# Kernel tuning notes

Hardware: AMD Instinct MI355X
Metric: run time of the kernel (lower is better)

## Reference

```python
import jax, jax.numpy as jnp
import numpy as np

T, B, N = 5, 1048576, 16
GAMMA = 0.99


def setup_inputs() -> dict:
    key = jax.random.key(0)
    k = jax.random.split(key, 6)
    q = jax.random.normal(k[0], (B, N), dtype=jnp.float32)
    next_n_q = jax.random.normal(k[1], (B, N), dtype=jnp.float32)
    action = jax.random.randint(k[2], (B,), 0, N)
    next_n_action = jax.random.randint(k[3], (B,), 0, N)
    reward = jax.random.normal(k[4], (T, B), dtype=jnp.float32)
    done = jax.random.randint(k[5], (B,), 0, 2).astype(jnp.bool_)
    weight = jnp.ones((B,), dtype=jnp.float32)
    gamma = jnp.float32(GAMMA)
    return {"q": q, "next_n_q": next_n_q, "action": action,
            "next_n_action": next_n_action, "reward": reward,
            "done": done, "weight": weight, "gamma": gamma}


def reference(q, next_n_q, action, next_n_action, reward, done, weight, gamma):
    # q, next_n_q: (B, N); action/next_n_action/done/weight: (B,); reward: (T, B)
    t = reward.shape[0]
    # gather Q(s,a) and Q(s_{t+n}, a') by action index
    q_s_a = jnp.take_along_axis(q, action[:, None], axis=1)[:, 0]            # (B,)
    next_q_s_a = jnp.take_along_axis(next_n_q, next_n_action[:, None], axis=1)[:, 0]
    # n-step discounted return: sum_t gamma^t r_t + gamma^T * Q' * (1 - done)
    factors = gamma ** jnp.arange(t, dtype=q.dtype)                          # (T,)
    not_done = 1.0 - done.astype(q.dtype)
    target = jnp.einsum('t,tb->b', factors, reward) + (gamma ** t) * next_q_s_a * not_done
    target = jax.lax.stop_gradient(target)
    # per-sample MSE td error, weighted mean loss
    td_error_per_sample = jnp.square(q_s_a - target)                         # (B,)
    loss = jnp.mean(td_error_per_sample * weight)                            # ()
    return loss, td_error_per_sample
```

## Files before the change

### kernel.cpp

```cpp
#include <hip/hip_runtime.h>


#define TILE_ROWS 512
#define BLOCK     256

__global__ __launch_bounds__(BLOCK) void qnstep_td_main(
    const float* __restrict__ q,
    const float* __restrict__ nq,
    const int*   __restrict__ act,
    const int*   __restrict__ nact,
    const float* __restrict__ rew,
    const int*   __restrict__ done,
    const float* __restrict__ w,
    const float* __restrict__ gamma_p,
    float*       __restrict__ out,
    float*       __restrict__ partial,
    int B, int T)
{
    __shared__ float tile[TILE_ROWS * 16];

    const int tid  = threadIdx.x;
    const long long base = (long long)blockIdx.x * TILE_ROWS;
    const float gamma = gamma_p[0];

    const long long g = base / 2 + tid;
    const int2   a2  = ((const int2*)act)[g];
    const int2   na2 = ((const int2*)nact)[g];
    const int2   d2  = ((const int2*)done)[g];
    const float2 w2  = ((const float2*)w)[g];

    float t0 = 0.f, t1 = 0.f, f = 1.0f;
    #pragma unroll 8
    for (int t = 0; t < T; ++t) {
        const float2 r2 = ((const float2*)(rew + (long long)t * B))[g];
        t0 += f * r2.x; t1 += f * r2.y;
        f *= gamma;
    }

    const int s0 = tid * 2, s1 = tid * 2 + 1;

    float4* t4 = (float4*)tile;
    {
        const float4* q4 = (const float4*)q + base * 4;
        #pragma unroll
        for (int j = 0; j < 8; ++j)
            t4[tid + j * BLOCK] = q4[tid + j * BLOCK];
    }
    __syncthreads();
    const float qa0 = tile[s0 * 16 + a2.x];
    const float qa1 = tile[s1 * 16 + a2.y];
    __syncthreads();

    {
        const float4* nq4 = (const float4*)nq + base * 4;
        #pragma unroll
        for (int j = 0; j < 8; ++j)
            t4[tid + j * BLOCK] = nq4[tid + j * BLOCK];
    }
    __syncthreads();
    const float nqa0 = tile[s0 * 16 + na2.x];
    const float nqa1 = tile[s1 * 16 + na2.y];

    t0 += f * nqa0 * (d2.x ? 0.f : 1.f);
    t1 += f * nqa1 * (d2.y ? 0.f : 1.f);
    const float e0 = qa0 - t0, e1 = qa1 - t1;
    const float td0 = e0 * e0, td1 = e1 * e1;

    out[1 + base + s0] = td0;
    out[1 + base + s1] = td1;

    float val = td0 * w2.x + td1 * w2.y;

    #pragma unroll
    for (int off = 32; off > 0; off >>= 1)
        val += __shfl_down(val, off, 64);

    __shared__ float ssum[BLOCK / 64];
    const int wave = tid >> 6, lane = tid & 63;
    if (lane == 0) ssum[wave] = val;
    __syncthreads();
    if (tid == 0) {
        float s = 0.f;
        #pragma unroll
        for (int i = 0; i < BLOCK / 64; ++i) s += ssum[i];
        partial[blockIdx.x] = s;
    }
}

__global__ __launch_bounds__(256) void qnstep_td_generic(
    const float* __restrict__ q, const float* __restrict__ nq,
    const int* __restrict__ act, const int* __restrict__ nact,
    const float* __restrict__ rew, const int* __restrict__ done,
    const float* __restrict__ w, const float* __restrict__ gamma_p,
    float* __restrict__ out, float* __restrict__ partial,
    int B, int N, int T)
{
    const int b = blockIdx.x * blockDim.x + threadIdx.x;
    const float gamma = gamma_p[0];
    float val = 0.0f;
    if (b < B) {
        float f = 1.0f, tgt = 0.0f;
        for (int t = 0; t < T; ++t) { tgt += f * rew[(long long)t * B + b]; f *= gamma; }
        const float nd = (done[b] != 0) ? 0.f : 1.f;
        tgt += f * nq[(long long)b * N + nact[b]] * nd;
        const float d = q[(long long)b * N + act[b]] - tgt;
        const float td = d * d;
        out[1 + b] = td;
        val = td * w[b];
    }
    #pragma unroll
    for (int off = 32; off > 0; off >>= 1) val += __shfl_down(val, off, 64);
    __shared__ float ssum[4];
    if ((threadIdx.x & 63) == 0) ssum[threadIdx.x >> 6] = val;
    __syncthreads();
    if (threadIdx.x == 0)
        partial[blockIdx.x] = ssum[0] + ssum[1] + ssum[2] + ssum[3];
}

__global__ __launch_bounds__(1024) void qnstep_td_reduce(
    const float* __restrict__ partial, float* __restrict__ out,
    int n, float invB)
{
    const int tid = threadIdx.x;
    float v = 0.0f;
    for (int i = tid; i < n; i += 1024) v += partial[i];

    #pragma unroll
    for (int off = 32; off > 0; off >>= 1)
        v += __shfl_down(v, off, 64);

    __shared__ float ssum[16];
    if ((tid & 63) == 0) ssum[tid >> 6] = v;
    __syncthreads();

    if (tid == 0) {
        float s = 0.0f;
        #pragma unroll
        for (int i = 0; i < 16; ++i) s += ssum[i];
        out[0] = s * invB;
    }
}

extern "C" void kernel_launch(void* const* d_in, const int* in_sizes, int n_in,
                              void* d_out, int out_size, void* d_ws, size_t ws_size,
                              hipStream_t stream) {
    const float* q     = (const float*)d_in[0];
    const float* nq    = (const float*)d_in[1];
    const int*   act   = (const int*)d_in[2];
    const int*   nact  = (const int*)d_in[3];
    const float* rew   = (const float*)d_in[4];
    const int*   done  = (const int*)d_in[5];
    const float* w     = (const float*)d_in[6];
    const float* gamma = (const float*)d_in[7];

    const int B = in_sizes[2];
    const int N = in_sizes[0] / B;
    const int T = in_sizes[4] / B;

    float* out     = (float*)d_out;
    float* partial = (float*)d_ws;

    if (N == 16 && (B % TILE_ROWS) == 0) {
        const int grid = B / TILE_ROWS;
        qnstep_td_main<<<grid, BLOCK, 0, stream>>>(
            q, nq, act, nact, rew, done, w, gamma, out, partial, B, T);
        qnstep_td_reduce<<<1, 1024, 0, stream>>>(partial, out, grid, 1.0f / (float)B);
    } else {
        const int grid = (B + 255) / 256;
        qnstep_td_generic<<<grid, 256, 0, stream>>>(
            q, nq, act, nact, rew, done, w, gamma, out, partial, B, N, T);
        qnstep_td_reduce<<<1, 1024, 0, stream>>>(partial, out, grid, 1.0f / (float)B);
    }
}
```

Measured before the change: 185.2 us.

## Gather only the needed float4 per row instead of staging full tiles in LDS

Replaces the shared-memory staging of full q and next_n_q rows with a direct float4 load of the 4-element chunk containing the selected action, then picks the element with selects. This cuts requested global traffic for the two large arrays and removes the LDS round trips and barriers. Reward loads are hoisted into a register array before accumulation, and an occupancy hint is added; the fast path now requires T <= 8. Scattered 16-byte loads may still pull whole cache sectors, which limits the traffic savings.

Measured after the change: 189.8 us. +2.5%, slower.

```diff
diff --git a/kernel.cpp b/kernel.cpp
--- a/kernel.cpp
+++ b/kernel.cpp
@@ -1,10 +1,9 @@
 #include <hip/hip_runtime.h>
 
 
-#define TILE_ROWS 512
-#define BLOCK     256
+#define BLOCK 256
 
-__global__ __launch_bounds__(BLOCK) void qnstep_td_main(
+__global__ __launch_bounds__(BLOCK, 8) void qnstep_td_main(
     const float* __restrict__ q,
     const float* __restrict__ nq,
     const int*   __restrict__ act,
@@ -17,57 +16,46 @@
     float*       __restrict__ partial,
     int B, int T)
 {
-    __shared__ float tile[TILE_ROWS * 16];
-
-    const int tid  = threadIdx.x;
-    const long long base = (long long)blockIdx.x * TILE_ROWS;
+    const int  g  = blockIdx.x * BLOCK + threadIdx.x;
+    const long long b0 = (long long)g * 2;
     const float gamma = gamma_p[0];
 
-    const long long g = base / 2 + tid;
     const int2   a2  = ((const int2*)act)[g];
     const int2   na2 = ((const int2*)nact)[g];
     const int2   d2  = ((const int2*)done)[g];
     const float2 w2  = ((const float2*)w)[g];
 
+    const float4 qv0  = *(const float4*)(q  + (b0 << 4)       + ((long long)(a2.x  >> 2) << 2));
+    const float4 qv1  = *(const float4*)(q  + ((b0 + 1) << 4) + ((long long)(a2.y  >> 2) << 2));
+    const float4 nqv0 = *(const float4*)(nq + (b0 << 4)       + ((long long)(na2.x >> 2) << 2));
+    const float4 nqv1 = *(const float4*)(nq + ((b0 + 1) << 4) + ((long long)(na2.y >> 2) << 2));
+
+    float2 r[8];
+    #pragma unroll 8
+    for (int t = 0; t < T; ++t)
+        r[t] = ((const float2*)(rew + (long long)t * B))[g];
+
     float t0 = 0.f, t1 = 0.f, f = 1.0f;
     #pragma unroll 8
     for (int t = 0; t < T; ++t) {
-        const float2 r2 = ((const float2*)(rew + (long long)t * B))[g];
-        t0 += f * r2.x; t1 += f * r2.y;
+        t0 += f * r[t].x; t1 += f * r[t].y;
         f *= gamma;
     }
 
-    const int s0 = tid * 2, s1 = tid * 2 + 1;
-
-    float4* t4 = (float4*)tile;
-    {
-        const float4* q4 = (const float4*)q + base * 4;
-        #pragma unroll
-        for (int j = 0; j < 8; ++j)
-            t4[tid + j * BLOCK] = q4[tid + j * BLOCK];
-    }
-    __syncthreads();
-    const float qa0 = tile[s0 * 16 + a2.x];
-    const float qa1 = tile[s1 * 16 + a2.y];
-    __syncthreads();
-
-    {
-        const float4* nq4 = (const float4*)nq + base * 4;
-        #pragma unroll
-        for (int j = 0; j < 8; ++j)
-            t4[tid + j * BLOCK] = nq4[tid + j * BLOCK];
-    }
-    __syncthreads();
-    const float nqa0 = tile[s0 * 16 + na2.x];
-    const float nqa1 = tile[s1 * 16 + na2.y];
+    const int c0 = a2.x & 3, c1 = a2.y & 3, c2 = na2.x & 3, c3 = na2.y & 3;
+    const float qa0  = (c0 < 2) ? (c0 == 0 ? qv0.x  : qv0.y)  : (c0 == 2 ? qv0.z  : qv0.w);
+    const float qa1  = (c1 < 2) ? (c1 == 0 ? qv1.x  : qv1.y)  : (c1 == 2 ? qv1.z  : qv1.w);
+    const float nqa0 = (c2 < 2) ? (c2 == 0 ? nqv0.x : nqv0.y) : (c2 == 2 ? nqv0.z : nqv0.w);
+    const float nqa1 = (c3 < 2) ? (c3 == 0 ? nqv1.x : nqv1.y) : (c3 == 2 ? nqv1.z : nqv1.w);
 
     t0 += f * nqa0 * (d2.x ? 0.f : 1.f);
     t1 += f * nqa1 * (d2.y ? 0.f : 1.f);
+
     const float e0 = qa0 - t0, e1 = qa1 - t1;
     const float td0 = e0 * e0, td1 = e1 * e1;
 
-    out[1 + base + s0] = td0;
-    out[1 + base + s1] = td1;
+    out[1 + b0]     = td0;
+    out[1 + b0 + 1] = td1;
 
     float val = td0 * w2.x + td1 * w2.y;
 
@@ -76,10 +64,9 @@
         val += __shfl_down(val, off, 64);
 
     __shared__ float ssum[BLOCK / 64];
-    const int wave = tid >> 6, lane = tid & 63;
-    if (lane == 0) ssum[wave] = val;
+    if ((threadIdx.x & 63) == 0) ssum[threadIdx.x >> 6] = val;
     __syncthreads();
-    if (tid == 0) {
+    if (threadIdx.x == 0) {
         float s = 0.f;
         #pragma unroll
         for (int i = 0; i < BLOCK / 64; ++i) s += ssum[i];
@@ -160,8 +147,8 @@
     float* out     = (float*)d_out;
     float* partial = (float*)d_ws;
 
-    if (N == 16 && (B % TILE_ROWS) == 0) {
-        const int grid = B / TILE_ROWS;
+    if (N == 16 && (B % (BLOCK * 2)) == 0 && T <= 8) {
+        const int grid = B / (BLOCK * 2);
         qnstep_td_main<<<grid, BLOCK, 0, stream>>>(
             q, nq, act, nact, rew, done, w, gamma, out, partial, B, T);
         qnstep_td_reduce<<<1, 1024, 0, stream>>>(partial, out, grid, 1.0f / (float)B);
```
